# Performance work log

Measured on AMD Instinct MI355X. Metric: run time of the kernel, lower is better.

## Reference

```python
import jax, jax.numpy as jnp
import numpy as np

B, LQ, LD, H, C = 128, 32, 512, 768, 128


def setup_inputs() -> dict:
    key = jax.random.key(0)
    ks = jax.random.split(key, 8)
    return {
        "query_hidden": jax.random.normal(ks[0], (B, LQ, H), dtype=jnp.float32),
        "doc_hidden": jax.random.normal(ks[1], (B, LD, H), dtype=jnp.float32),
        "query_mask": jax.random.randint(ks[2], (B, LQ), 0, 2, dtype=jnp.int32),
        "doc_mask": jax.random.randint(ks[3], (B, LD), 0, 2, dtype=jnp.int32),
        "W_comp": jax.random.normal(ks[4], (H, C), dtype=jnp.float32) * (1.0 / np.sqrt(H)),
        "b_comp": jax.random.normal(ks[5], (C,), dtype=jnp.float32) * 0.02,
        "w_stop": jax.random.normal(ks[6], (C, 1), dtype=jnp.float32) * (1.0 / np.sqrt(C)),
        "b_stop": jnp.ones((1,), dtype=jnp.float32),  # nn.init.constant_(bias, 1)
        "score_merger": jnp.zeros((1,), dtype=jnp.float32),
    }


def reference(query_hidden, doc_hidden, query_mask, doc_mask,
              W_comp, b_comp, w_stop, b_stop, score_merger):
    qm = query_mask.astype(bool)  # [B, LQ]
    dm = doc_mask.astype(bool)    # [B, LD]

    # encode_shared: CLS vec is the UNcompressed hidden state at position 0
    q_cls = query_hidden[:, 0, :]  # [B, H]
    d_cls = doc_hidden[:, 0, :]    # [B, H]

    # compressor (Linear H->C)
    q_vecs = jnp.einsum('blh,hc->blc', query_hidden, W_comp) + b_comp  # [B, LQ, C]
    d_tok = jnp.einsum('blh,hc->blc', doc_hidden, W_comp) + b_comp     # [B, LD, C]

    # encode_query: zero masked query tokens
    q_vecs = q_vecs * qm[..., None]

    # encode_doc: stopword reducer (relu of Linear C->1), then importance + mask
    importance = jax.nn.relu(jnp.einsum('blc,co->blo', d_tok, w_stop) + b_stop)  # [B, LD, 1]
    d_vecs = d_tok * importance * dm[..., None]

    # CLS score: dot product of (uncompressed) CLS vectors
    cls_score = jnp.sum(q_cls * d_cls, axis=-1)  # [B]

    # term score: MaxSim over doc tokens, masked sum over query tokens
    scores = jnp.einsum('bqc,bkc->bqk', q_vecs, d_vecs)      # [B, LQ, LD]
    scores = jnp.where(dm[:, None, :], scores, -1000.0)
    term = jnp.max(scores, axis=-1)                          # [B, LQ]
    term_score = jnp.sum(jnp.where(qm, term, 0.0), axis=-1)  # [B]

    w = jax.nn.sigmoid(score_merger[0])
    cls_score = cls_score * w
    term_score = term_score * (1.0 - w)
    score = cls_score + term_score
    return (score, cls_score, term_score)
```

## Files before the change

kernel.cpp:

```cpp
#include <hip/hip_runtime.h>
#include <hip/hip_bf16.h>

#define Bb 128
#define LQ 32
#define LD 512
#define Hh 768
#define Cc 128

#define DBLOCKS ((Bb * LD) / 64)

typedef short bf16x8 __attribute__((ext_vector_type(8)));
typedef short bf16x4 __attribute__((ext_vector_type(4)));
typedef float f32x4 __attribute__((ext_vector_type(4)));

__device__ __forceinline__ short f2bf(float f) {
  union { float f; unsigned u; } v;
  v.f = f;
  unsigned u = v.u + (0x7FFFu + ((v.u >> 16) & 1u));
  return (short)(u >> 16);
}

__device__ __forceinline__ float b2f(short s) {
  union { unsigned u; float f; } v;
  v.u = ((unsigned)(unsigned short)s) << 16;
  return v.f;
}

__global__ __launch_bounds__(256) void k_wt(const float* __restrict__ W,
                                            short* __restrict__ Wt) {
  int idx = blockIdx.x * 256 + threadIdx.x;
  int h = idx >> 7;
  int c = idx & 127;
  Wt[c * Hh + h] = f2bf(W[idx]);
}

__global__ __launch_bounds__(256, 4) void k_fused(
    const float* __restrict__ dh, const float* __restrict__ qh,
    const short* __restrict__ Wt, const float* __restrict__ bcomp,
    const int* __restrict__ qmask, const int* __restrict__ dmask,
    const float* __restrict__ wstop, const float* __restrict__ bstop,
    float* __restrict__ partial) {
  constexpr int ASTR = 144;
  constexpr int BSTR = 160;
  constexpr int ASZ = 64 * ASTR;
  constexpr int SSTR = 136;
  constexpr int NK = Hh / 64;
  __shared__ __align__(16) char smem[29696 + 256 + 512];

  char* bufA = smem;
  char* bufB = smem + ASZ;
  short* dvt = (short*)smem;
  short* lqt = (short*)(smem + 17408);
  int* dmsk = (int*)(smem + 29696);
  float* pm = (float*)(smem + 29696 + 256);

  const int tid = threadIdx.x;
  const int w = tid >> 6;
  const int lane = tid & 63;
  const int quad = lane >> 4;
  const int lm = lane & 15;
  const bool isq = (w < 2);

  const int b = blockIdx.x >> 3;
  const int chunk = blockIdx.x & 7;
  const long row0b = (long)b * LD + chunk * 64;

  if (tid < 64) dmsk[tid] = dmask[row0b + tid];

  const float* gA = dh + (row0b + w * 16 + (lane >> 4)) * (long)Hh + (lane & 15) * 4;
  const short* gB = Wt + (w * 32 + (lane >> 3)) * Hh + (lane & 7) * 8;
  const float* gQ = qh + ((long)b * LQ + w * 16 + lm) * Hh + quad * 8;
  const int aoff = (w * 16 + (lane >> 4)) * ASTR + (lane & 15) * 8;
  const int boff = (w * 32 + (lane >> 3)) * BSTR + (lane & 7) * 16;

  f32x4 acc[8], accq[8];
#pragma unroll
  for (int j = 0; j < 8; ++j) acc[j] = (f32x4){0.f, 0.f, 0.f, 0.f};
#pragma unroll
  for (int j = 0; j < 8; ++j) accq[j] = (f32x4){0.f, 0.f, 0.f, 0.f};

  float4 ar[4], aq[4];
  bf16x8 br[4];
#pragma unroll
  for (int i = 0; i < 4; ++i) ar[i] = *(const float4*)(gA + i * 4 * Hh);
#pragma unroll
  for (int i = 0; i < 4; ++i) br[i] = *(const bf16x8*)(gB + i * 8 * Hh);
  if (isq) {
#pragma unroll
    for (int i = 0; i < 4; ++i)
      aq[i] = *(const float4*)(gQ + (i >> 1) * 32 + (i & 1) * 4);
  }

  for (int kk = 0; kk < NK; ++kk) {
    __syncthreads();
#pragma unroll
    for (int i = 0; i < 4; ++i) {
      bf16x4 p;
      p[0] = f2bf(ar[i].x); p[1] = f2bf(ar[i].y);
      p[2] = f2bf(ar[i].z); p[3] = f2bf(ar[i].w);
      *(bf16x4*)(bufA + aoff + i * 4 * ASTR) = p;
    }
#pragma unroll
    for (int i = 0; i < 4; ++i)
      *(bf16x8*)(bufB + boff + i * 8 * BSTR) = br[i];
    __syncthreads();

    bf16x8 fq0, fq1;
    if (isq) {
      fq0[0] = f2bf(aq[0].x); fq0[1] = f2bf(aq[0].y);
      fq0[2] = f2bf(aq[0].z); fq0[3] = f2bf(aq[0].w);
      fq0[4] = f2bf(aq[1].x); fq0[5] = f2bf(aq[1].y);
      fq0[6] = f2bf(aq[1].z); fq0[7] = f2bf(aq[1].w);
      fq1[0] = f2bf(aq[2].x); fq1[1] = f2bf(aq[2].y);
      fq1[2] = f2bf(aq[2].z); fq1[3] = f2bf(aq[2].w);
      fq1[4] = f2bf(aq[3].x); fq1[5] = f2bf(aq[3].y);
      fq1[6] = f2bf(aq[3].z); fq1[7] = f2bf(aq[3].w);
    }

    {
      const long go = (kk + 1 < NK) ? (long)(kk + 1) * 64 : 0;
#pragma unroll
      for (int i = 0; i < 4; ++i) ar[i] = *(const float4*)(gA + i * 4 * Hh + go);
#pragma unroll
      for (int i = 0; i < 4; ++i) br[i] = *(const bf16x8*)(gB + i * 8 * Hh + go);
      if (isq) {
#pragma unroll
        for (int i = 0; i < 4; ++i)
          aq[i] = *(const float4*)(gQ + go + (i >> 1) * 32 + (i & 1) * 4);
      }
    }

#pragma unroll
    for (int ks = 0; ks < 2; ++ks) {
      bf16x8 fa = *(const bf16x8*)(bufA + (w * 16 + lm) * ASTR + ks * 64 + quad * 16);
      const bf16x8 fqk = (ks == 0) ? fq0 : fq1;
#pragma unroll
      for (int j = 0; j < 8; ++j) {
        bf16x8 fb = *(const bf16x8*)(bufB + (j * 16 + lm) * BSTR + ks * 64 + quad * 16);
        acc[j] = __builtin_amdgcn_mfma_f32_16x16x32_bf16(fa, fb, acc[j], 0, 0, 0);
        if (isq)
          accq[j] = __builtin_amdgcn_mfma_f32_16x16x32_bf16(fqk, fb, accq[j], 0, 0, 0);
      }
    }
  }

  __syncthreads();

  float bc[8], wsv[8];
#pragma unroll
  for (int j = 0; j < 8; ++j) bc[j] = bcomp[j * 16 + lm];
#pragma unroll
  for (int j = 0; j < 8; ++j) wsv[j] = wstop[j * 16 + lm];
  const float bs = bstop[0];

#pragma unroll
  for (int r = 0; r < 4; ++r) {
    const int lrow = w * 16 + quad * 4 + r;
    float v[8];
#pragma unroll
    for (int j = 0; j < 8; ++j) v[j] = acc[j][r] + bc[j];
    float p = 0.f;
#pragma unroll
    for (int j = 0; j < 8; ++j) p += v[j] * wsv[j];
    p += __shfl_xor(p, 1);
    p += __shfl_xor(p, 2);
    p += __shfl_xor(p, 4);
    p += __shfl_xor(p, 8);
    const float imp = fmaxf(p + bs, 0.f);
    const float scale = imp * (float)dmsk[lrow];
#pragma unroll
    for (int j = 0; j < 8; ++j)
      dvt[lrow * SSTR + j * 16 + lm] = f2bf(v[j] * scale);
  }
  if (isq) {
    const int qrow0 = w * 16 + quad * 4;
#pragma unroll
    for (int r = 0; r < 4; ++r) {
      const int qrow = qrow0 + r;
      const float scale = (float)qmask[b * LQ + qrow];
#pragma unroll
      for (int j = 0; j < 8; ++j)
        lqt[qrow * SSTR + j * 16 + lm] = f2bf((accq[j][r] + bc[j]) * scale);
    }
  }
  __syncthreads();

  const int qt = tid & 15;
  const int kt = tid >> 4;
  const int kbase = kt * 4;
  float a[2][4];
#pragma unroll
  for (int qi = 0; qi < 2; ++qi)
#pragma unroll
    for (int ki = 0; ki < 4; ++ki) a[qi][ki] = 0.f;

  for (int c = 0; c < Cc; c += 8) {
    bf16x8 q0 = *(const bf16x8*)&lqt[qt * SSTR + c];
    bf16x8 q1 = *(const bf16x8*)&lqt[(qt + 16) * SSTR + c];
    bf16x8 d0 = *(const bf16x8*)&dvt[(kbase + 0) * SSTR + c];
    bf16x8 d1 = *(const bf16x8*)&dvt[(kbase + 1) * SSTR + c];
    bf16x8 d2 = *(const bf16x8*)&dvt[(kbase + 2) * SSTR + c];
    bf16x8 d3 = *(const bf16x8*)&dvt[(kbase + 3) * SSTR + c];
#pragma unroll
    for (int e = 0; e < 8; ++e) {
      const float f0 = b2f(q0[e]);
      const float f1 = b2f(q1[e]);
      const float g0 = b2f(d0[e]);
      const float g1 = b2f(d1[e]);
      const float g2 = b2f(d2[e]);
      const float g3 = b2f(d3[e]);
      a[0][0] += f0 * g0; a[0][1] += f0 * g1;
      a[0][2] += f0 * g2; a[0][3] += f0 * g3;
      a[1][0] += f1 * g0; a[1][1] += f1 * g1;
      a[1][2] += f1 * g2; a[1][3] += f1 * g3;
    }
  }
  float m0 = -1000.f, m1 = -1000.f;
#pragma unroll
  for (int ki = 0; ki < 4; ++ki) {
    if (dmsk[kbase + ki]) {
      m0 = fmaxf(m0, a[0][ki]);
      m1 = fmaxf(m1, a[1][ki]);
    }
  }
  m0 = fmaxf(m0, __shfl_xor(m0, 16));
  m0 = fmaxf(m0, __shfl_xor(m0, 32));
  m1 = fmaxf(m1, __shfl_xor(m1, 16));
  m1 = fmaxf(m1, __shfl_xor(m1, 32));
  if (lane < 16) {
    pm[w * 32 + lane] = m0;
    pm[w * 32 + lane + 16] = m1;
  }
  __syncthreads();
  if (tid < LQ) {
    float mx = fmaxf(fmaxf(pm[tid], pm[32 + tid]),
                     fmaxf(pm[64 + tid], pm[96 + tid]));
    partial[((size_t)b * LQ + tid) * 8 + chunk] = mx;
  }
}

__global__ __launch_bounds__(256) void k_final(
    const float* __restrict__ qh, const float* __restrict__ dh,
    const int* __restrict__ qmask, const float* __restrict__ partial,
    const float* __restrict__ merger, float* __restrict__ out) {
  const int b = blockIdx.x;
  const int tid = threadIdx.x;
  __shared__ float red[256];
  __shared__ float clss;
  const float* qc = qh + (size_t)b * LQ * Hh;
  const float* dc = dh + (size_t)b * LD * Hh;
  float s = 0.f;
  for (int h = tid; h < Hh; h += 256) s += qc[h] * dc[h];
  red[tid] = s;
  __syncthreads();
  for (int off = 128; off > 0; off >>= 1) {
    if (tid < off) red[tid] += red[tid + off];
    __syncthreads();
  }
  if (tid == 0) clss = red[0];
  __syncthreads();
  float t = 0.f;
  if (tid < LQ) {
    const float* pp = partial + ((size_t)b * LQ + tid) * 8;
    float mx = pp[0];
#pragma unroll
    for (int c = 1; c < 8; ++c) mx = fmaxf(mx, pp[c]);
    if (qmask[b * LQ + tid]) t = mx;
  }
  red[tid] = t;
  __syncthreads();
  for (int off = 128; off > 0; off >>= 1) {
    if (tid < off) red[tid] += red[tid + off];
    __syncthreads();
  }
  if (tid == 0) {
    float w = 1.f / (1.f + expf(-merger[0]));
    float cs = clss * w;
    float ts = red[0] * (1.f - w);
    out[b] = cs + ts;
    out[Bb + b] = cs;
    out[2 * Bb + b] = ts;
  }
}

extern "C" void kernel_launch(void* const* d_in, const int* in_sizes, int n_in,
                              void* d_out, int out_size, void* d_ws, size_t ws_size,
                              hipStream_t stream) {
  const float* qh  = (const float*)d_in[0];
  const float* dh  = (const float*)d_in[1];
  const int*   qm  = (const int*)d_in[2];
  const int*   dm  = (const int*)d_in[3];
  const float* W   = (const float*)d_in[4];
  const float* bc  = (const float*)d_in[5];
  const float* wst = (const float*)d_in[6];
  const float* bst = (const float*)d_in[7];
  const float* mrg = (const float*)d_in[8];
  float* out = (float*)d_out;

  char* ws = (char*)d_ws;
  short* Wt  = (short*)ws;
  float* prt = (float*)(ws + 196608);

  k_wt<<<(Hh * Cc) / 256, 256, 0, stream>>>(W, Wt);
  k_fused<<<DBLOCKS, 256, 0, stream>>>(dh, qh, Wt, bc, qm, dm, wst, bst, prt);
  k_final<<<Bb, 256, 0, stream>>>(qh, dh, qm, prt, mrg, out);
}
```

Baseline: 360.1 us.

## Split query projection into its own kernel and stream W fragments from global

Moves the query compression out of the doc kernel into a separate k_proj_q kernel that writes masked fp32 query vectors once per batch. Previously every one of the 8 doc-chunk blocks per batch recomputed the query projection. The doc kernel now loads W fragments straight from global/L2 instead of staging them in LDS, double-buffers the A loads in registers two k-steps ahead, and drops a barrier pair. This removes redundant MFMA work and shrinks LDS use, but adds an extra launch plus workspace traffic, and W is now read from cache by every wave.

```diff
diff --git a/kernel.cpp b/kernel.cpp
--- a/kernel.cpp
+++ b/kernel.cpp
@@ -8,6 +8,7 @@
 #define Cc 128
 
 #define DBLOCKS ((Bb * LD) / 64)
+#define QBLOCKS ((Bb * LQ) / 64)
 
 typedef short bf16x8 __attribute__((ext_vector_type(8)));
 typedef short bf16x4 __attribute__((ext_vector_type(4)));
@@ -34,64 +35,44 @@
   Wt[c * Hh + h] = f2bf(W[idx]);
 }
 
-__global__ __launch_bounds__(256, 4) void k_fused(
-    const float* __restrict__ dh, const float* __restrict__ qh,
-    const short* __restrict__ Wt, const float* __restrict__ bcomp,
-    const int* __restrict__ qmask, const int* __restrict__ dmask,
-    const float* __restrict__ wstop, const float* __restrict__ bstop,
-    float* __restrict__ partial) {
+__global__ __launch_bounds__(256, 4) void k_proj_q(
+    const float* __restrict__ qh, const short* __restrict__ Wt,
+    const float* __restrict__ bcomp, const int* __restrict__ qmask,
+    float* __restrict__ qv) {
   constexpr int ASTR = 144;
   constexpr int BSTR = 160;
   constexpr int ASZ = 64 * ASTR;
-  constexpr int SSTR = 136;
-  constexpr int NK = Hh / 64;
-  __shared__ __align__(16) char smem[29696 + 256 + 512];
-
-  char* bufA = smem;
-  char* bufB = smem + ASZ;
-  short* dvt = (short*)smem;
-  short* lqt = (short*)(smem + 17408);
-  int* dmsk = (int*)(smem + 29696);
-  float* pm = (float*)(smem + 29696 + 256);
+  constexpr int BSZ = 128 * BSTR;
+  __shared__ __align__(16) char sm[ASZ + BSZ];
 
   const int tid = threadIdx.x;
   const int w = tid >> 6;
   const int lane = tid & 63;
   const int quad = lane >> 4;
   const int lm = lane & 15;
-  const bool isq = (w < 2);
-
-  const int b = blockIdx.x >> 3;
-  const int chunk = blockIdx.x & 7;
-  const long row0b = (long)b * LD + chunk * 64;
-
-  if (tid < 64) dmsk[tid] = dmask[row0b + tid];
-
-  const float* gA = dh + (row0b + w * 16 + (lane >> 4)) * (long)Hh + (lane & 15) * 4;
+
+  const long row0b = (long)blockIdx.x * 64;
+
+  const float* gA = qh + (row0b + w * 16 + (lane >> 4)) * (long)Hh + (lane & 15) * 4;
   const short* gB = Wt + (w * 32 + (lane >> 3)) * Hh + (lane & 7) * 8;
-  const float* gQ = qh + ((long)b * LQ + w * 16 + lm) * Hh + quad * 8;
   const int aoff = (w * 16 + (lane >> 4)) * ASTR + (lane & 15) * 8;
   const int boff = (w * 32 + (lane >> 3)) * BSTR + (lane & 7) * 16;
 
-  f32x4 acc[8], accq[8];
+  char* bufA = sm;
+  char* bufB = sm + ASZ;
+
+  f32x4 acc[8];
 #pragma unroll
   for (int j = 0; j < 8; ++j) acc[j] = (f32x4){0.f, 0.f, 0.f, 0.f};
-#pragma unroll
-  for (int j = 0; j < 8; ++j) accq[j] = (f32x4){0.f, 0.f, 0.f, 0.f};
-
-  float4 ar[4], aq[4];
+
+  float4 ar[4];
   bf16x8 br[4];
 #pragma unroll
   for (int i = 0; i < 4; ++i) ar[i] = *(const float4*)(gA + i * 4 * Hh);
 #pragma unroll
   for (int i = 0; i < 4; ++i) br[i] = *(const bf16x8*)(gB + i * 8 * Hh);
-  if (isq) {
-#pragma unroll
-    for (int i = 0; i < 4; ++i)
-      aq[i] = *(const float4*)(gQ + (i >> 1) * 32 + (i & 1) * 4);
-  }
-
-  for (int kk = 0; kk < NK; ++kk) {
+
+  for (int kk = 0; kk < Hh / 64; ++kk) {
     __syncthreads();
 #pragma unroll
     for (int i = 0; i < 4; ++i) {
@@ -105,46 +86,130 @@
       *(bf16x8*)(bufB + boff + i * 8 * BSTR) = br[i];
     __syncthreads();
 
-    bf16x8 fq0, fq1;
-    if (isq) {
-      fq0[0] = f2bf(aq[0].x); fq0[1] = f2bf(aq[0].y);
-      fq0[2] = f2bf(aq[0].z); fq0[3] = f2bf(aq[0].w);
-      fq0[4] = f2bf(aq[1].x); fq0[5] = f2bf(aq[1].y);
-      fq0[6] = f2bf(aq[1].z); fq0[7] = f2bf(aq[1].w);
-      fq1[0] = f2bf(aq[2].x); fq1[1] = f2bf(aq[2].y);
-      fq1[2] = f2bf(aq[2].z); fq1[3] = f2bf(aq[2].w);
-      fq1[4] = f2bf(aq[3].x); fq1[5] = f2bf(aq[3].y);
-      fq1[6] = f2bf(aq[3].z); fq1[7] = f2bf(aq[3].w);
-    }
-
     {
-      const long go = (kk + 1 < NK) ? (long)(kk + 1) * 64 : 0;
+      const long go = (kk + 1 < Hh / 64) ? (long)(kk + 1) * 64 : 0;
 #pragma unroll
       for (int i = 0; i < 4; ++i) ar[i] = *(const float4*)(gA + i * 4 * Hh + go);
 #pragma unroll
       for (int i = 0; i < 4; ++i) br[i] = *(const bf16x8*)(gB + i * 8 * Hh + go);
-      if (isq) {
-#pragma unroll
-        for (int i = 0; i < 4; ++i)
-          aq[i] = *(const float4*)(gQ + go + (i >> 1) * 32 + (i & 1) * 4);
-      }
     }
 
 #pragma unroll
     for (int ks = 0; ks < 2; ++ks) {
       bf16x8 fa = *(const bf16x8*)(bufA + (w * 16 + lm) * ASTR + ks * 64 + quad * 16);
-      const bf16x8 fqk = (ks == 0) ? fq0 : fq1;
 #pragma unroll
       for (int j = 0; j < 8; ++j) {
         bf16x8 fb = *(const bf16x8*)(bufB + (j * 16 + lm) * BSTR + ks * 64 + quad * 16);
         acc[j] = __builtin_amdgcn_mfma_f32_16x16x32_bf16(fa, fb, acc[j], 0, 0, 0);
-        if (isq)
-          accq[j] = __builtin_amdgcn_mfma_f32_16x16x32_bf16(fqk, fb, accq[j], 0, 0, 0);
       }
     }
   }
 
-  __syncthreads();
+  const long row0 = row0b + w * 16;
+  float bc[8];
+#pragma unroll
+  for (int j = 0; j < 8; ++j) bc[j] = bcomp[j * 16 + lm];
+
+#pragma unroll
+  for (int r = 0; r < 4; ++r) {
+    const long row = row0 + quad * 4 + r;
+    const float scale = (float)qmask[row];
+    float* yr = qv + row * Cc;
+#pragma unroll
+    for (int j = 0; j < 8; ++j) yr[j * 16 + lm] = (acc[j][r] + bc[j]) * scale;
+  }
+}
+
+__global__ __launch_bounds__(256, 4) void k_fused(
+    const float* __restrict__ dh, const short* __restrict__ Wt,
+    const float* __restrict__ qv, const float* __restrict__ bcomp,
+    const int* __restrict__ dmask, const float* __restrict__ wstop,
+    const float* __restrict__ bstop, float* __restrict__ partial) {
+  constexpr int ASTR = 144;
+  constexpr int SSTR = 136;
+  constexpr int NK = Hh / 64;
+  __shared__ __align__(16) char smem[26112 + 256 + 512];
+
+  char* bufA = smem;
+  short* dvt = (short*)smem;
+  short* lqt = (short*)(smem + 17408);
+  int* dmsk = (int*)(smem + 26112);
+  float* pm = (float*)(smem + 26112 + 256);
+
+  const int tid = threadIdx.x;
+  const int w = tid >> 6;
+  const int lane = tid & 63;
+  const int quad = lane >> 4;
+  const int lm = lane & 15;
+
+  const int b = blockIdx.x >> 3;
+  const int chunk = blockIdx.x & 7;
+  const long row0b = (long)b * LD + chunk * 64;
+
+  if (tid < 64) dmsk[tid] = dmask[row0b + tid];
+
+  const float* gA = dh + (row0b + w * 16 + (lane >> 4)) * (long)Hh + (lane & 15) * 4;
+  const short* gB = Wt + lm * Hh + quad * 8;
+  const int aoff = (w * 16 + (lane >> 4)) * ASTR + (lane & 15) * 8;
+
+  f32x4 acc[8];
+#pragma unroll
+  for (int j = 0; j < 8; ++j) acc[j] = (f32x4){0.f, 0.f, 0.f, 0.f};
+
+  float4 arA[4], arB[4];
+#pragma unroll
+  for (int i = 0; i < 4; ++i) arA[i] = *(const float4*)(gA + i * 4 * Hh);
+#pragma unroll
+  for (int i = 0; i < 4; ++i) arB[i] = *(const float4*)(gA + 64 + i * 4 * Hh);
+
+  auto iter = [&](int kk, float4 (&ar)[4]) {
+#pragma unroll
+    for (int i = 0; i < 4; ++i) {
+      bf16x4 p;
+      p[0] = f2bf(ar[i].x); p[1] = f2bf(ar[i].y);
+      p[2] = f2bf(ar[i].z); p[3] = f2bf(ar[i].w);
+      *(bf16x4*)(bufA + aoff + i * 4 * ASTR) = p;
+    }
+#pragma unroll
+    for (int ks = 0; ks < 2; ++ks) {
+      bf16x8 fa = *(const bf16x8*)(bufA + (w * 16 + lm) * ASTR + ks * 64 + quad * 16);
+      bf16x8 fbv[8];
+#pragma unroll
+      for (int j = 0; j < 8; ++j)
+        fbv[j] = *(const bf16x8*)(gB + j * 16 * Hh + kk * 64 + ks * 32);
+#pragma unroll
+      for (int j = 0; j < 8; ++j)
+        acc[j] = __builtin_amdgcn_mfma_f32_16x16x32_bf16(fa, fbv[j], acc[j], 0, 0, 0);
+    }
+    const long go = (kk + 2 < NK) ? (long)(kk + 2) * 64 : 0;
+#pragma unroll
+    for (int i = 0; i < 4; ++i)
+      ar[i] = *(const float4*)(gA + go + i * 4 * Hh);
+  };
+
+  for (int kp = 0; kp < NK / 2; ++kp) {
+    iter(2 * kp, arA);
+    iter(2 * kp + 1, arB);
+  }
+
+  __syncthreads();
+
+  {
+    const float4* src = (const float4*)(qv + (size_t)b * LQ * Cc);
+    float4 t[4];
+#pragma unroll
+    for (int k = 0; k < 4; ++k) t[k] = src[tid + k * 256];
+#pragma unroll
+    for (int k = 0; k < 4; ++k) {
+      const int i = tid + k * 256;
+      const int q = i >> 5;
+      const int c = (i & 31) << 2;
+      bf16x4 p;
+      p[0] = f2bf(t[k].x); p[1] = f2bf(t[k].y);
+      p[2] = f2bf(t[k].z); p[3] = f2bf(t[k].w);
+      *(bf16x4*)&lqt[q * SSTR + c] = p;
+    }
+  }
 
   float bc[8], wsv[8];
 #pragma unroll
@@ -171,17 +236,6 @@
 #pragma unroll
     for (int j = 0; j < 8; ++j)
       dvt[lrow * SSTR + j * 16 + lm] = f2bf(v[j] * scale);
-  }
-  if (isq) {
-    const int qrow0 = w * 16 + quad * 4;
-#pragma unroll
-    for (int r = 0; r < 4; ++r) {
-      const int qrow = qrow0 + r;
-      const float scale = (float)qmask[b * LQ + qrow];
-#pragma unroll
-      for (int j = 0; j < 8; ++j)
-        lqt[qrow * SSTR + j * 16 + lm] = f2bf((accq[j][r] + bc[j]) * scale);
-    }
   }
   __syncthreads();
 
@@ -299,9 +353,11 @@
 
   char* ws = (char*)d_ws;
   short* Wt  = (short*)ws;
-  float* prt = (float*)(ws + 196608);
+  float* qv  = (float*)(ws + 196608);
+  float* prt = (float*)(ws + 196608 + 2097152);
 
   k_wt<<<(Hh * Cc) / 256, 256, 0, stream>>>(W, Wt);
-  k_fused<<<DBLOCKS, 256, 0, stream>>>(dh, qh, Wt, bc, qm, dm, wst, bst, prt);
+  k_proj_q<<<QBLOCKS, 256, 0, stream>>>(qh, Wt, bc, qm, qv);
+  k_fused<<<DBLOCKS, 256, 0, stream>>>(dh, Wt, qv, bc, dm, wst, bst, prt);
   k_final<<<Bb, 256, 0, stream>>>(qh, dh, qm, prt, mrg, out);
 }
```

New measurement: 388.4 us. 7.8% more time.
